# Kernel tuning notes

Measured on AMD Instinct MI355X. Metric: run time of the kernel, lower is better.

## Reference

```python
import jax, jax.numpy as jnp
import numpy as np

INPUT_SIZE = 9
HIDDEN = 50
OUTPUT = 1


def setup_inputs() -> dict:
    key = jax.random.key(0)
    ks = jax.random.split(key, 7)
    B, T = 4096, 512
    s_ih = 1.0 / np.sqrt(HIDDEN)
    inp = {
        "x": jax.random.normal(ks[0], (B, T, INPUT_SIZE), dtype=jnp.float32),
        # PyTorch LSTM params, gate order [i, f, g, o]
        "w_ih": jax.random.uniform(ks[1], (4 * HIDDEN, INPUT_SIZE), minval=-s_ih, maxval=s_ih, dtype=jnp.float32),
        "w_hh": jax.random.uniform(ks[2], (4 * HIDDEN, HIDDEN), minval=-s_ih, maxval=s_ih, dtype=jnp.float32),
        "b_ih": jax.random.uniform(ks[3], (4 * HIDDEN,), minval=-s_ih, maxval=s_ih, dtype=jnp.float32),
        "b_hh": jax.random.uniform(ks[4], (4 * HIDDEN,), minval=-s_ih, maxval=s_ih, dtype=jnp.float32),
        "fc_w": jax.random.uniform(ks[5], (OUTPUT, HIDDEN), minval=-s_ih, maxval=s_ih, dtype=jnp.float32),
        "fc_b": jax.random.uniform(ks[6], (OUTPUT,), minval=-s_ih, maxval=s_ih, dtype=jnp.float32),
    }
    return inp


def _lstm_last_h(x, w_ih, w_hh, b_ih, b_hh):
    B, T, _ = x.shape
    H = w_hh.shape[1]
    # Precompute input-side gate pre-activations for all timesteps: [T, B, 4H]
    x_gates = jnp.einsum("bti,gi->tbg", x, w_ih) + (b_ih + b_hh)

    def step(carry, xg):
        h, c = carry
        gates = xg + h @ w_hh.T  # [B, 4H]
        i, f, g, o = jnp.split(gates, 4, axis=-1)
        i = jax.nn.sigmoid(i)
        f = jax.nn.sigmoid(f)
        g = jnp.tanh(g)
        o = jax.nn.sigmoid(o)
        c = f * c + i * g
        h = o * jnp.tanh(c)
        return (h, c), None

    h0 = jnp.zeros((B, H), dtype=x.dtype)
    c0 = jnp.zeros((B, H), dtype=x.dtype)
    (h_last, _), _ = jax.lax.scan(step, (h0, c0), x_gates)
    return h_last


def reference(x, w_ih, w_hh, b_ih, b_hh, fc_w, fc_b):
    h_last = _lstm_last_h(x, w_ih, w_hh, b_ih, b_hh)  # [B, H]
    return h_last @ fc_w.T + fc_b  # [B, 1]
```

## Files before the change

### kernel.cpp

```cpp
#include <hip/hip_runtime.h>
#include <hip/hip_bf16.h>

#define TT    512
#define ISZ   9
#define HH    50
#define NB    16
#define NWAVE 16
#define NTH   (NWAVE * 64)
#define KDIM  64

typedef __bf16 bf16x8_t __attribute__((ext_vector_type(8)));
typedef float  f32x4_t  __attribute__((ext_vector_type(4)));

#define L2E  1.44269504088896340736f

#define BAR() asm volatile("s_waitcnt lgkmcnt(0)\n\ts_barrier" ::: "memory")

__device__ __forceinline__ unsigned short bf16_rne(float f) {
  unsigned u = __builtin_bit_cast(unsigned, f);
  unsigned r = (u + 0x7FFFu + ((u >> 16) & 1u)) >> 16;
  return (unsigned short)r;
}
__device__ __forceinline__ unsigned short bf16h(float v) {
  __bf16 b = (__bf16)v;
  return __builtin_bit_cast(unsigned short, b);
}
__device__ __forceinline__ float sg_exp2(float z) { return __builtin_amdgcn_exp2f(z); }
__device__ __forceinline__ float rcp_f(float z)   { return __builtin_amdgcn_rcpf(z); }

__global__ __launch_bounds__(NTH, 1) void lstm_mfma(
    const float* __restrict__ x,
    const float* __restrict__ w_ih,
    const float* __restrict__ w_hh,
    const float* __restrict__ b_ih,
    const float* __restrict__ b_hh,
    const float* __restrict__ fc_w,
    const float* __restrict__ fc_b,
    float* __restrict__ out) {
  __shared__ __align__(16) unsigned short hbuf[2][NB * KDIM];
  __shared__ float redbuf[NWAVE][NB];

  const int tid = threadIdx.x;
  const int w   = tid >> 6;
  const int l   = tid & 63;
  const int lb  = l & 15;
  const int kq  = l >> 4;
  const int b0  = blockIdx.x * NB;
  const bool cw = (w < 13);

  for (int i = tid; i < (2 * NB * KDIM) / 2; i += NTH)
    reinterpret_cast<unsigned*>(hbuf)[i] = 0u;

  const int xt = tid - 13 * 64;
  const bool xact = (xt >= 0 && xt < NB * ISZ);
  const int xb = xact ? (xt / ISZ) : 0;
  const int xi = xact ? (xt - xb * ISZ) : 0;
  __syncthreads();
  if (xact) {
    float xv = x[(size_t)(b0 + xb) * (TT * ISZ) + xi];
    *(unsigned short*)((char*)hbuf[0] + (((xb << 7) + ((50 + xi) << 1)) ^ ((xb & 7) << 4))) = bf16h(xv);
  }

  bf16x8_t afrag[2];
  {
    const int rp   = w * 16 + lb;
    const int jA   = rp >> 2;
    const int gA   = rp & 3;
    const int rowA = gA * HH + jA;
    const bool liveA = cw && (jA < HH);
    const float scA = (gA == 2) ? (2.0f * L2E) : (-L2E);
#pragma unroll
    for (int ks = 0; ks < 2; ++ks) {
#pragma unroll
      for (int e = 0; e < 8; ++e) {
        const int K = ks * 32 + kq * 8 + e;
        unsigned short bits = 0;
        if (liveA) {
          if (K < HH)                 bits = bf16_rne(w_hh[rowA * HH + K] * scA);
          else if (K < HH + ISZ)      bits = bf16_rne(w_ih[rowA * ISZ + (K - HH)] * scA);
        }
        afrag[ks][e] = __builtin_bit_cast(__bf16, bits);
      }
    }
  }

  const int j0 = w * 4 + kq;
  const bool live0 = cw && (j0 < HH);
  f32x4_t bias0 = {0.f, 0.f, 0.f, 0.f};
  if (live0) {
#pragma unroll
    for (int r = 0; r < 4; ++r) {
      const float sc = (r == 2) ? (2.0f * L2E) : (-L2E);
      bias0[r] = (b_ih[r * HH + j0] + b_hh[r * HH + j0]) * sc;
    }
  }

  char* const base = (char*)hbuf[0];
  const int swzb = (lb & 7) << 4;
  const int rd0 = ((lb << 7) + 0  + (kq << 4)) ^ swzb;
  const int rd1 = ((lb << 7) + 64 + (kq << 4)) ^ swzb;
  const int j0c = (j0 < HH) ? j0 : (j0 + 9);
  const int wo0 = (((lb << 7) + (j0c << 1)) ^ swzb);
  const int xwo = (((xb << 7) + ((50 + xi) << 1)) ^ ((xb & 7) << 4));

  const float* xp = x + (size_t)(b0 + xb) * (TT * ISZ) + xi;
  float csc = 0.0f, h0 = 0.0f;
  float xv_n = 0.0f;
  if (xact) xv_n = xp[ISZ];
  xp += 2 * ISZ;

#define STEP(T, ROFF, WOFF)                                                      \
  if (cw) {                                                                      \
    BAR();                                                                       \
    bf16x8_t bb0 = *(const bf16x8_t*)(base + rd0 + (ROFF));                      \
    bf16x8_t bb1 = *(const bf16x8_t*)(base + rd1 + (ROFF));                      \
    f32x4_t acc;                                                                 \
    acc = __builtin_amdgcn_mfma_f32_16x16x32_bf16(afrag[0], bb0, bias0, 0,0,0);  \
    acc = __builtin_amdgcn_mfma_f32_16x16x32_bf16(afrag[1], bb1, acc,   0,0,0);  \
    const float pi = sg_exp2(acc[0]);                                \
    const float pf = sg_exp2(acc[1]);                                \
    const float eg = sg_exp2(acc[2]);                                \
    const float po = sg_exp2(acc[3]);                                \
    const float r1 = rcp_f((1.0f + pi) * (1.0f + eg));                           \
    const float fv = rcp_f(1.0f + pf);                                           \
    const float ig2 = (eg - 1.0f) * r1 * (2.0f * L2E);                           \
    csc = fmaf(fv, csc, ig2);                                 \
    const float ec = sg_exp2(csc);                                               \
    const float r2 = rcp_f((1.0f + po) * (1.0f + ec));                           \
    h0 = (ec - 1.0f) * r2;                                                       \
    *(unsigned short*)(base + wo0 + (WOFF)) = bf16h(h0);                         \
  } else {                                                                       \
    float xv_new = 0.0f;                                                         \
    if (xact && (T) + 2 < TT) xv_new = *xp;                                      \
    xp += ISZ;                                                                   \
    BAR();                                                                       \
    if (xact && (T) + 1 < TT) *(unsigned short*)(base + xwo + (WOFF)) = bf16h(xv_n); \
    xv_n = xv_new;                                                               \
  }

  for (int t2 = 0; t2 < TT; t2 += 2) {
    STEP(t2,     0x000, 0x800);
    STEP(t2 + 1, 0x800, 0x000);
  }
#undef STEP

  float p = live0 ? h0 * fc_w[j0] : 0.0f;
  p += __shfl_xor(p, 16);
  p += __shfl_xor(p, 32);
  if (l < NB) redbuf[w][l] = p;
  __syncthreads();
  if (tid < NB) {
    float a = fc_b[0];
#pragma unroll
    for (int ww = 0; ww < NWAVE; ++ww) a += redbuf[ww][tid];
    out[b0 + tid] = a;
  }
}

extern "C" void kernel_launch(void* const* d_in, const int* in_sizes, int n_in,
                              void* d_out, int out_size, void* d_ws, size_t ws_size,
                              hipStream_t stream) {
  const float* x    = (const float*)d_in[0];
  const float* w_ih = (const float*)d_in[1];
  const float* w_hh = (const float*)d_in[2];
  const float* b_ih = (const float*)d_in[3];
  const float* b_hh = (const float*)d_in[4];
  const float* fc_w = (const float*)d_in[5];
  const float* fc_b = (const float*)d_in[6];
  float* out = (float*)d_out;
  const int Btot = in_sizes[0] / (TT * ISZ);
  dim3 grid(Btot / NB), block(NTH);
  hipLaunchKernelGGL(lstm_mfma, grid, block, 0, stream,
                     x, w_ih, w_hh, b_ih, b_hh, fc_w, fc_b, out);
}
```

Before: 183.4 us.

## Switch LSTM MFMA to fp16, shrink to 14 waves, merge reciprocals, add setprio

Switches the recurrent matmul operands from bf16 to fp16 (more mantissa, same MFMA shape). It cuts the block from 16 to 14 waves by having one wave (48 lanes × 3) stage all 144 x values per step, so fewer waves join each barrier. The three sigmoid/tanh reciprocals merge into one shared reciprocal, and s_setprio is raised around the MFMA section. The gains would come from cheaper per-step barrier sync and fewer transcendental ops on the serial critical path. The cost is heavier loading work on the single x-staging wave and possible fp16 overflow in the merged product.

```diff
diff --git a/kernel.cpp b/kernel.cpp
--- a/kernel.cpp
+++ b/kernel.cpp
@@ -5,24 +5,20 @@
 #define ISZ   9
 #define HH    50
 #define NB    16
-#define NWAVE 16
+#define NWAVE 14
 #define NTH   (NWAVE * 64)
 #define KDIM  64
 
-typedef __bf16 bf16x8_t __attribute__((ext_vector_type(8)));
-typedef float  f32x4_t  __attribute__((ext_vector_type(4)));
+typedef _Float16 f16x8_t __attribute__((ext_vector_type(8)));
+typedef float    f32x4_t __attribute__((ext_vector_type(4)));
 
-#define L2E  1.44269504088896340736f
+#define L2E   1.44269504088896340736f
+#define TWOL2E 2.88539008177792681472f
 
 #define BAR() asm volatile("s_waitcnt lgkmcnt(0)\n\ts_barrier" ::: "memory")
 
-__device__ __forceinline__ unsigned short bf16_rne(float f) {
-  unsigned u = __builtin_bit_cast(unsigned, f);
-  unsigned r = (u + 0x7FFFu + ((u >> 16) & 1u)) >> 16;
-  return (unsigned short)r;
-}
-__device__ __forceinline__ unsigned short bf16h(float v) {
-  __bf16 b = (__bf16)v;
+__device__ __forceinline__ unsigned short f16h(float v) {
+  _Float16 b = (_Float16)v;
   return __builtin_bit_cast(unsigned short, b);
 }
 __device__ __forceinline__ float sg_exp2(float z) { return __builtin_amdgcn_exp2f(z); }
@@ -51,35 +47,43 @@
   for (int i = tid; i < (2 * NB * KDIM) / 2; i += NTH)
     reinterpret_cast<unsigned*>(hbuf)[i] = 0u;
 
-  const int xt = tid - 13 * 64;
-  const bool xact = (xt >= 0 && xt < NB * ISZ);
-  const int xb = xact ? (xt / ISZ) : 0;
-  const int xi = xact ? (xt - xb * ISZ) : 0;
+  const bool sw = (w == 13) && (l < 48);
+  int xb_[3], xi_[3], xwo_[3];
+  const float* xp_[3];
+#pragma unroll
+  for (int k = 0; k < 3; ++k) {
+    const int e = l + 48 * k;
+    xb_[k] = sw ? (e / ISZ) : 0;
+    xi_[k] = sw ? (e - xb_[k] * ISZ) : 0;
+    xwo_[k] = (((xb_[k] << 7) + ((50 + xi_[k]) << 1)) ^ ((xb_[k] & 7) << 4));
+    xp_[k] = x + (size_t)(b0 + xb_[k]) * (TT * ISZ) + xi_[k];
+  }
   __syncthreads();
-  if (xact) {
-    float xv = x[(size_t)(b0 + xb) * (TT * ISZ) + xi];
-    *(unsigned short*)((char*)hbuf[0] + (((xb << 7) + ((50 + xi) << 1)) ^ ((xb & 7) << 4))) = bf16h(xv);
+  if (sw) {
+#pragma unroll
+    for (int k = 0; k < 3; ++k)
+      *(unsigned short*)((char*)hbuf[0] + xwo_[k]) = f16h(*xp_[k]);
   }
 
-  bf16x8_t afrag[2];
+  f16x8_t afrag[2];
   {
     const int rp   = w * 16 + lb;
     const int jA   = rp >> 2;
     const int gA   = rp & 3;
     const int rowA = gA * HH + jA;
     const bool liveA = cw && (jA < HH);
-    const float scA = (gA == 2) ? (2.0f * L2E) : (-L2E);
+    const float scA = (gA == 2) ? TWOL2E : (-L2E);
 #pragma unroll
     for (int ks = 0; ks < 2; ++ks) {
 #pragma unroll
       for (int e = 0; e < 8; ++e) {
         const int K = ks * 32 + kq * 8 + e;
-        unsigned short bits = 0;
+        float v = 0.0f;
         if (liveA) {
-          if (K < HH)                 bits = bf16_rne(w_hh[rowA * HH + K] * scA);
-          else if (K < HH + ISZ)      bits = bf16_rne(w_ih[rowA * ISZ + (K - HH)] * scA);
+          if (K < HH)            v = w_hh[rowA * HH + K] * scA;
+          else if (K < HH + ISZ) v = w_ih[rowA * ISZ + (K - HH)] * scA;
         }
-        afrag[ks][e] = __builtin_bit_cast(__bf16, bits);
+        afrag[ks][e] = (_Float16)v;
       }
     }
   }
@@ -90,7 +94,7 @@
   if (live0) {
 #pragma unroll
     for (int r = 0; r < 4; ++r) {
-      const float sc = (r == 2) ? (2.0f * L2E) : (-L2E);
+      const float sc = (r == 2) ? TWOL2E : (-L2E);
       bias0[r] = (b_ih[r * HH + j0] + b_hh[r * HH + j0]) * sc;
     }
   }
@@ -101,41 +105,52 @@
   const int rd1 = ((lb << 7) + 64 + (kq << 4)) ^ swzb;
   const int j0c = (j0 < HH) ? j0 : (j0 + 9);
   const int wo0 = (((lb << 7) + (j0c << 1)) ^ swzb);
-  const int xwo = (((xb << 7) + ((50 + xi) << 1)) ^ ((xb & 7) << 4));
 
-  const float* xp = x + (size_t)(b0 + xb) * (TT * ISZ) + xi;
   float csc = 0.0f, h0 = 0.0f;
-  float xv_n = 0.0f;
-  if (xact) xv_n = xp[ISZ];
-  xp += 2 * ISZ;
+  float xv_n[3] = {0.f, 0.f, 0.f};
+  if (sw) {
+#pragma unroll
+    for (int k = 0; k < 3; ++k) { xv_n[k] = xp_[k][ISZ]; xp_[k] += 2 * ISZ; }
+  }
 
 #define STEP(T, ROFF, WOFF)                                                      \
   if (cw) {                                                                      \
     BAR();                                                                       \
-    bf16x8_t bb0 = *(const bf16x8_t*)(base + rd0 + (ROFF));                      \
-    bf16x8_t bb1 = *(const bf16x8_t*)(base + rd1 + (ROFF));                      \
+    __builtin_amdgcn_s_setprio(1);                                               \
+    f16x8_t bb0 = *(const f16x8_t*)(base + rd0 + (ROFF));                        \
+    f16x8_t bb1 = *(const f16x8_t*)(base + rd1 + (ROFF));                        \
     f32x4_t acc;                                                                 \
-    acc = __builtin_amdgcn_mfma_f32_16x16x32_bf16(afrag[0], bb0, bias0, 0,0,0);  \
-    acc = __builtin_amdgcn_mfma_f32_16x16x32_bf16(afrag[1], bb1, acc,   0,0,0);  \
+    acc = __builtin_amdgcn_mfma_f32_16x16x32_f16(afrag[0], bb0, bias0, 0,0,0);   \
+    acc = __builtin_amdgcn_mfma_f32_16x16x32_f16(afrag[1], bb1, acc,   0,0,0);   \
+    __builtin_amdgcn_s_setprio(0);                                               \
     const float pi = sg_exp2(acc[0]);                                \
     const float pf = sg_exp2(acc[1]);                                \
     const float eg = sg_exp2(acc[2]);                                \
     const float po = sg_exp2(acc[3]);                                \
-    const float r1 = rcp_f((1.0f + pi) * (1.0f + eg));                           \
-    const float fv = rcp_f(1.0f + pf);                                           \
-    const float ig2 = (eg - 1.0f) * r1 * (2.0f * L2E);                           \
+    const float A1 = 1.0f + pi, A2 = 1.0f + eg, A3 = 1.0f + pf;                  \
+    const float P  = A1 * A2;                                                    \
+    const float R  = rcp_f(P * A3);                                              \
+    const float u  = (eg - 1.0f) * TWOL2E;                                       \
+    const float fv = P * R;                                        \
+    const float ig2 = u * (A3 * R);                              \
     csc = fmaf(fv, csc, ig2);                                 \
     const float ec = sg_exp2(csc);                                               \
     const float r2 = rcp_f((1.0f + po) * (1.0f + ec));                           \
     h0 = (ec - 1.0f) * r2;                                                       \
-    *(unsigned short*)(base + wo0 + (WOFF)) = bf16h(h0);                         \
+    *(unsigned short*)(base + wo0 + (WOFF)) = f16h(h0);                          \
   } else {                                                                       \
-    float xv_new = 0.0f;                                                         \
-    if (xact && (T) + 2 < TT) xv_new = *xp;                                      \
-    xp += ISZ;                                                                   \
+    float xnew[3] = {0.f, 0.f, 0.f};                                             \
+    if (sw && (T) + 2 < TT) {                                                    \
+      xnew[0] = *xp_[0]; xnew[1] = *xp_[1]; xnew[2] = *xp_[2];                   \
+    }                                                                            \
+    if (sw) { xp_[0] += ISZ; xp_[1] += ISZ; xp_[2] += ISZ; }                     \
     BAR();                                                                       \
-    if (xact && (T) + 1 < TT) *(unsigned short*)(base + xwo + (WOFF)) = bf16h(xv_n); \
-    xv_n = xv_new;                                                               \
+    if (sw && (T) + 1 < TT) {                                                    \
+      *(unsigned short*)(base + xwo_[0] + (WOFF)) = f16h(xv_n[0]);               \
+      *(unsigned short*)(base + xwo_[1] + (WOFF)) = f16h(xv_n[1]);               \
+      *(unsigned short*)(base + xwo_[2] + (WOFF)) = f16h(xv_n[2]);               \
+    }                                                                            \
+    xv_n[0] = xnew[0]; xv_n[1] = xnew[1]; xv_n[2] = xnew[2];                     \
   }
 
   for (int t2 = 0; t2 < TT; t2 += 2) {
```

After: 202.0 us. 10.1% more time.
